# Optimization experiments

Measured on AMD Instinct MI355X. Metric: run time of the kernel, lower is better.

Reference implementation:

```python
import jax, jax.numpy as jnp
import numpy as np

SEQ, NV, NH, NR = 32768, 256, 512, 256


def _bern(key, p):
    # torch.bernoulli: sample is non-differentiable
    return (jax.random.uniform(key, p.shape, dtype=p.dtype) < p).astype(p.dtype)


def setup_inputs() -> dict:
    key = jax.random.key(0)
    ks = jax.random.split(key, 8)
    f32 = jnp.float32
    return {
        "v_seq": (jax.random.uniform(ks[0], (SEQ, NV), dtype=f32) < 0.1).astype(f32),
        "W1": jax.random.normal(ks[1], (NV, NH), dtype=f32) * 0.01,
        "bv": jnp.zeros((NV,), f32),
        "bh1": jnp.zeros((NH,), f32),
        "W2": jax.random.normal(ks[2], (NH, NH), dtype=f32) * 0.01,
        "bh2": jnp.zeros((NH,), f32),
        "Wyv": jax.random.normal(ks[3], (NV, NR), dtype=f32) * 1e-4,
        "Wyh1": jax.random.normal(ks[4], (NH, NR), dtype=f32) * 1e-4,
        "Wyh2": jax.random.normal(ks[5], (NH, NR), dtype=f32) * 1e-4,
        "Wvu": jax.random.normal(ks[6], (NV, NR), dtype=f32) * 0.01,
        "Wuu": jax.random.normal(ks[7], (NR, NR), dtype=f32) * 0.01,
        "bu": jnp.zeros((NR,), f32),
        "k": 5,
    }


def reference(v_seq, W1, bv, bh1, W2, bh2, Wyv, Wyh1, Wyh2, Wvu, Wuu, bu, k):
    dtype = v_seq.dtype
    nr = Wuu.shape[0]
    seq_len = v_seq.shape[0]

    # vanilla tanh RNN (abstract _run_rnn in base class)
    def rnn_step(u, v):
        u_new = jnp.tanh(v @ Wvu + u @ Wuu + bu)
        return u_new, u_new

    _, rnn_out = jax.lax.scan(rnn_step, jnp.zeros((nr,), dtype), v_seq)
    shifted = jnp.concatenate([jnp.zeros((1, nr), dtype), rnn_out[:-1]], axis=0)

    bv_t = bv + shifted @ Wyv.T    # [S, NV]
    bh1_t = bh1 + shifted @ Wyh1.T  # [S, NH]
    bh2_t = bh2 + shifted @ Wyh2.T  # [S, NH]

    key = jax.random.key(42)

    # CD-k Gibbs chain, RBM1 (visible <-> hidden1)
    v_sample = v_seq
    mean_v = None
    for _ in range(k):
        key, k1, k2 = jax.random.split(key, 3)
        h = _bern(k1, jax.nn.sigmoid(v_sample @ W1 + bh1_t))
        mean_v = jax.nn.sigmoid(h @ W1.T + bv_t)
        v_sample = _bern(k2, mean_v)

    def free_energy1(v):
        return -(v * bv_t).sum(-1) - jax.nn.softplus(v @ W1 + bh1_t).sum(-1)

    cost1 = (free_energy1(v_seq) - free_energy1(jax.lax.stop_gradient(v_sample))).mean()

    # CD-k Gibbs chain, RBM2 (hidden1 <-> hidden2)
    h1 = jax.nn.sigmoid(v_seq @ W1 + bh1_t)
    h1_sample = h1
    for _ in range(k):
        key, k1, k2 = jax.random.split(key, 3)
        h2 = _bern(k1, jax.nn.sigmoid(h1_sample @ W2 + bh2_t))
        h1_sample = _bern(k2, jax.nn.sigmoid(h2 @ W2.T + bh1_t))

    def free_energy2(h):
        return -(h * bh1_t).sum(-1) - jax.nn.softplus(h @ W2 + bh2_t).sum(-1)

    cost2 = (free_energy2(h1) - free_energy2(jax.lax.stop_gradient(h1_sample))).mean()

    eps = 1e-10
    monitor = (v_seq * jnp.log(mean_v + eps)
               + (1.0 - v_seq) * jnp.log(1.0 - mean_v + eps)).sum() / seq_len
    return (cost1 + cost2, monitor)
```

## Files before the change

kernel.cpp:

```cpp
#include <hip/hip_runtime.h>
#include <cstdint>

#define S_LEN 32768
#define NV 256
#define NH 512
#define NR 256

typedef short bf16x8 __attribute__((ext_vector_type(8)));
typedef float f32x4 __attribute__((ext_vector_type(4)));
typedef unsigned short ushort_t;

__device__ __forceinline__ float b2f(ushort_t u) {
  return __uint_as_float(((uint32_t)u) << 16);
}
__device__ __forceinline__ ushort_t f2b(float f) {
  uint32_t x = __float_as_uint(f);
  uint32_t r = (x + 0x7fffu + ((x >> 16) & 1u)) >> 16;
  return (ushort_t)r;
}

#define GLOAD_LDS16(gsrc, ldst)                                        \
  __builtin_amdgcn_global_load_lds(                                    \
      (const __attribute__((address_space(1))) void*)(gsrc),           \
      (__attribute__((address_space(3))) void*)(ldst), 16, 0, 0)

#define TFR(x0,x1,r) { x0 += x1; x1 = ((x1 << (r)) | (x1 >> (32 - (r)))); x1 ^= x0; }
__host__ __forceinline__ void tf2x32(uint32_t k0, uint32_t k1,
                                     uint32_t x0, uint32_t x1,
                                     uint32_t* o0, uint32_t* o1) {
  uint32_t k2 = k0 ^ k1 ^ 0x1BD11BDAu;
  x0 += k0; x1 += k1;
  TFR(x0,x1,13) TFR(x0,x1,15) TFR(x0,x1,26) TFR(x0,x1,6)
  x0 += k1; x1 += k2 + 1u;
  TFR(x0,x1,17) TFR(x0,x1,29) TFR(x0,x1,16) TFR(x0,x1,24)
  x0 += k2; x1 += k0 + 2u;
  TFR(x0,x1,13) TFR(x0,x1,15) TFR(x0,x1,26) TFR(x0,x1,6)
  x0 += k0; x1 += k1 + 3u;
  TFR(x0,x1,17) TFR(x0,x1,29) TFR(x0,x1,16) TFR(x0,x1,24)
  x0 += k1; x1 += k2 + 4u;
  TFR(x0,x1,13) TFR(x0,x1,15) TFR(x0,x1,26) TFR(x0,x1,6)
  x0 += k2; x1 += k0 + 5u;
  *o0 = x0; *o1 = x1;
}

__device__ __forceinline__ uint32_t fast_hash(uint32_t k0, uint32_t k1, uint32_t idx) {
  uint32_t h = idx ^ k0;
  h *= 0xCC9E2D51u; h = (h << 15) | (h >> 17); h *= 0x1B873593u;
  h ^= k1;
  h ^= h >> 16; h *= 0x85EBCA6Bu;
  h ^= h >> 13; h *= 0xC2B2AE35u;
  h ^= h >> 16;
  return h;
}

__device__ __forceinline__ float wave_reduce(float v) {
#pragma unroll
  for (int o = 32; o > 0; o >>= 1) v += __shfl_down(v, o, 64);
  return v;
}
__device__ __forceinline__ float softplusf(float z) {
  return fmaxf(z, 0.f) + log1pf(expf(-fabsf(z)));
}

#define F_SAMP  4
#define F_H1    8
#define F_FE    16
#define F_MON   32
#define F_DOTB  64
#define F_DOTS  128
#define F_DOTV  256

struct GemmArgs {
  const ushort_t* A;
  const ushort_t* BT;
  const ushort_t* Ax;
  const ushort_t* BXT;
  const float* bvec;
  ushort_t* C;
  ushort_t* C2;
  const float* vseqf;
  double* fe_acc;
  double* mon_acc;
  float sign;
  uint32_t rk0, rk1;
  int N, K, nbx;
};

__device__ __forceinline__ void xcd_swz(int* bx, int* by) {
  const int gx = (int)gridDim.x;
  const int lin = (int)blockIdx.y * gx + (int)blockIdx.x;
  const int cpx = (gx * (int)gridDim.y) >> 3;
  const int w = (lin & 7) * cpx + (lin >> 3);
  const int lg = 31 - __clz(gx);
  *by = w >> lg;
  *bx = w & (gx - 1);
}

template<int FLAGS>
__device__ __forceinline__ void run_gemm(const GemmArgs& g, int bx, int by,
                                         ushort_t* __restrict__ As0,
                                         ushort_t* __restrict__ As1,
                                         ushort_t* __restrict__ Bs0,
                                         ushort_t* __restrict__ Bs1) {
  constexpr bool HASB = (FLAGS & (F_DOTB | F_DOTS | F_DOTV)) != 0;
  const int tid = threadIdx.x;
  const int lane = tid & 63, wave = tid >> 6;
  const int wm = wave >> 1, wn = wave & 1;
  const int q = lane >> 4, l16 = lane & 15;
  const int m0 = by * 128, n0 = bx * 128;
  const int N = g.N, K = g.K;
  const int KT = K + 256;

  f32x4 acc[4][4];
  f32x4 accB[4][4];
#pragma unroll
  for (int mt = 0; mt < 4; mt++)
#pragma unroll
    for (int nt = 0; nt < 4; nt++) {
      acc[mt][nt] = (f32x4){0.f, 0.f, 0.f, 0.f};
      if constexpr (HASB) accB[mt][nt] = (f32x4){0.f, 0.f, 0.f, 0.f};
    }

  auto stage = [&](ushort_t* As, ushort_t* Bs, int kks) {
    const ushort_t* Ap; const ushort_t* Bp; size_t lda; int k0;
    if (kks < K) { Ap = g.A;  Bp = g.BT;  lda = (size_t)K; k0 = kks; }
    else         { Ap = g.Ax; Bp = g.BXT; lda = 256;       k0 = kks - K; }
#pragma unroll
    for (int j = 0; j < 4; j++) {
      int c = j * 256 + tid;
      int r = c >> 3, bl = c & 7, bg = bl ^ (r & 7);
      (void)bl;
      const int ldso = (j * 256 + wave * 64) * 8;
      GLOAD_LDS16(&Ap[(size_t)(m0 + r) * lda + k0 + bg * 8], &As[ldso]);
      GLOAD_LDS16(&Bp[(size_t)(n0 + r) * lda + k0 + bg * 8], &Bs[ldso]);
    }
  };
  auto compute_into = [&](f32x4 (&ac)[4][4], const ushort_t* As, const ushort_t* Bs) {
#pragma unroll
    for (int c = 0; c < 2; c++) {
      bf16x8 af[4], bf[4];
#pragma unroll
      for (int mt = 0; mt < 4; mt++) {
        int r = wm * 64 + mt * 16 + l16;
        af[mt] = *(const bf16x8*)&As[r * 64 + (((c * 4 + q) ^ (r & 7)) * 8)];
      }
#pragma unroll
      for (int nt = 0; nt < 4; nt++) {
        int r = wn * 64 + nt * 16 + l16;
        bf[nt] = *(const bf16x8*)&Bs[r * 64 + (((c * 4 + q) ^ (r & 7)) * 8)];
      }
#pragma unroll
      for (int mt = 0; mt < 4; mt++)
#pragma unroll
        for (int nt = 0; nt < 4; nt++)
          ac[mt][nt] = __builtin_amdgcn_mfma_f32_16x16x32_bf16(
              af[mt], bf[nt], ac[mt][nt], 0, 0, 0);
    }
  };

  stage(As0, Bs0, 0);
  __syncthreads();
  for (int kk = 0; kk < KT; kk += 128) {
    stage(As1, Bs1, kk + 64);
    if (HASB && kk >= K) compute_into(accB, As0, Bs0);
    else                 compute_into(acc,  As0, Bs0);
    __syncthreads();
    if (kk + 128 < KT) stage(As0, Bs0, kk + 128);
    if (HASB && (kk + 64) >= K) compute_into(accB, As1, Bs1);
    else                        compute_into(acc,  As1, Bs1);
    __syncthreads();
  }

  float fe_sum = 0.f, mon_sum = 0.f;
#pragma unroll
  for (int mt = 0; mt < 4; mt++) {
#pragma unroll
    for (int nt = 0; nt < 4; nt++) {
      const int gn = n0 + wn * 64 + nt * 16 + l16;
      const int gmb = m0 + wm * 64 + mt * 16 + q * 4;
      const float bvv = g.bvec[gn];
      uint32_t h0 = 0, h1 = 0;
      if constexpr (FLAGS & F_SAMP) {
        uint32_t pb = (uint32_t)((gmb >> 1) * N + gn);
        h0 = fast_hash(g.rk0, g.rk1, pb);
        h1 = fast_hash(g.rk0, g.rk1, pb + (uint32_t)N);
      }
#pragma unroll
      for (int rg = 0; rg < 4; rg++) {
        const int gm = gmb + rg;
        const size_t idx = (size_t)gm * N + gn;
        float z, be = 0.f;
        if constexpr (HASB) {
          be = accB[mt][nt][rg] + bvv;
          z = acc[mt][nt][rg] + be;
        } else {
          z = acc[mt][nt][rg] + bvv;
        }
        if constexpr (FLAGS & F_DOTV) fe_sum += be * g.vseqf[idx];
        if constexpr (FLAGS & (F_SAMP | F_H1 | F_MON)) {
          float e = __expf(-z);
          if constexpr (FLAGS & F_SAMP) {
            uint32_t hb = (rg & 2) ? h1 : h0;
            uint32_t ub = (rg & 1) ? (hb >> 16) : (hb & 0xffffu);
            float uu = (float)ub * (1.0f / 65536.0f);
            bool sbit = fmaf(uu, e, uu) < 1.f;
            g.C[idx] = sbit ? (ushort_t)0x3f80 : (ushort_t)0;
            if constexpr (FLAGS & F_DOTS) fe_sum += sbit ? be : 0.f;
          }
          if constexpr (FLAGS & (F_H1 | F_MON)) {
            float pp = __builtin_amdgcn_rcpf(1.f + e);
            if constexpr (FLAGS & F_H1) g.C2[idx] = f2b(pp);
            if constexpr (FLAGS & F_DOTB) fe_sum += pp * be;
            if constexpr (FLAGS & F_MON) {
              float v = g.vseqf[idx];
              mon_sum += (v != 0.f) ? logf(pp + 1e-10f) : logf(1.f - pp + 1e-10f);
            }
          }
        }
        if constexpr (FLAGS & F_FE) fe_sum += softplusf(z);
      }
    }
  }
  if constexpr (FLAGS & (F_FE | F_DOTB | F_DOTS | F_DOTV)) {
    float s = wave_reduce(fe_sum);
    if (lane == 0) atomicAdd(g.fe_acc, (double)(-g.sign * s));
  }
  if constexpr (FLAGS & F_MON) {
    float s = wave_reduce(mon_sum);
    if (lane == 0) atomicAdd(g.mon_acc, (double)s);
  }
}

template<int FLAGS>
__global__ __launch_bounds__(256)
void gemm_samp(GemmArgs g) {
  __shared__ ushort_t As0[128 * 64], As1[128 * 64];
  __shared__ ushort_t Bs0[128 * 64], Bs1[128 * 64];
  int bx, by;
  xcd_swz(&bx, &by);
  if (bx >= g.nbx) return;
  run_gemm<FLAGS>(g, bx, by, As0, As1, Bs0, Bs1);
}

template<int F0, int F1>
__global__ __launch_bounds__(256)
void gemm_pair(GemmArgs g0, GemmArgs g1) {
  __shared__ ushort_t As0[128 * 64], As1[128 * 64];
  __shared__ ushort_t Bs0[128 * 64], Bs1[128 * 64];
  int bx, by;
  xcd_swz(&bx, &by);
  if (blockIdx.z == 0) {
    if (bx >= g0.nbx) return;
    run_gemm<F0>(g0, bx, by, As0, As1, Bs0, Bs1);
  } else {
    if (bx >= g1.nbx) return;
    run_gemm<F1>(g1, bx, by, As0, As1, Bs0, Bs1);
  }
}

__global__ __launch_bounds__(256)
void gemm_bias(const ushort_t* __restrict__ A, const ushort_t* __restrict__ BT,
               const float* __restrict__ biasv, float* __restrict__ Cf,
               int M, int N, int K) {
  __shared__ ushort_t As0[128 * 64], As1[128 * 64];
  __shared__ ushort_t Bs0[128 * 64], Bs1[128 * 64];
  const int tid = threadIdx.x;
  const int lane = tid & 63, wave = tid >> 6;
  const int wm = wave >> 1, wn = wave & 1;
  const int q = lane >> 4, l16 = lane & 15;
  int bx, by;
  xcd_swz(&bx, &by);
  const int m0 = by * 128, n0 = bx * 128;
  (void)lane;

  f32x4 acc[4][4];
#pragma unroll
  for (int i = 0; i < 4; i++)
#pragma unroll
    for (int j = 0; j < 4; j++) acc[i][j] = (f32x4){0.f, 0.f, 0.f, 0.f};

  auto stage = [&](ushort_t* As, ushort_t* Bs, int kk) {
#pragma unroll
    for (int j = 0; j < 4; j++) {
      int c = j * 256 + tid;
      int r = c >> 3, bl = c & 7, bg = bl ^ (r & 7);
      (void)bl;
      const int ldso = (j * 256 + wave * 64) * 8;
      GLOAD_LDS16(&A[(size_t)(m0 + r) * K + kk + bg * 8], &As[ldso]);
      GLOAD_LDS16(&BT[(size_t)(n0 + r) * K + kk + bg * 8], &Bs[ldso]);
    }
  };
  auto compute = [&](const ushort_t* As, const ushort_t* Bs) {
#pragma unroll
    for (int c = 0; c < 2; c++) {
      bf16x8 af[4], bf[4];
#pragma unroll
      for (int mt = 0; mt < 4; mt++) {
        int r = wm * 64 + mt * 16 + l16;
        af[mt] = *(const bf16x8*)&As[r * 64 + (((c * 4 + q) ^ (r & 7)) * 8)];
      }
#pragma unroll
      for (int nt = 0; nt < 4; nt++) {
        int r = wn * 64 + nt * 16 + l16;
        bf[nt] = *(const bf16x8*)&Bs[r * 64 + (((c * 4 + q) ^ (r & 7)) * 8)];
      }
#pragma unroll
      for (int mt = 0; mt < 4; mt++)
#pragma unroll
        for (int nt = 0; nt < 4; nt++)
          acc[mt][nt] = __builtin_amdgcn_mfma_f32_16x16x32_bf16(
              af[mt], bf[nt], acc[mt][nt], 0, 0, 0);
    }
  };

  stage(As0, Bs0, 0);
  __syncthreads();
  for (int kk = 0; kk < K; kk += 128) {
    stage(As1, Bs1, kk + 64);
    compute(As0, Bs0);
    __syncthreads();
    if (kk + 128 < K) stage(As0, Bs0, kk + 128);
    compute(As1, Bs1);
    __syncthreads();
  }

#pragma unroll
  for (int mt = 0; mt < 4; mt++)
#pragma unroll
    for (int nt = 0; nt < 4; nt++) {
      const int gn = n0 + wn * 64 + nt * 16 + l16;
      const int gmb = m0 + wm * 64 + mt * 16 + q * 4;
      const float bvv = biasv[gn];
#pragma unroll
      for (int rg = 0; rg < 4; rg++)
        Cf[(size_t)(gmb + rg) * N + gn] = acc[mt][nt][rg] + bvv;
    }
}

__global__ __launch_bounds__(1024, 1)
void rnn_scan(const float* __restrict__ Apre, const float* __restrict__ Wuu,
              ushort_t* __restrict__ shifted) {
  const int tid = threadIdx.x;
  const int j = tid >> 2;
  const int s = tid & 3;
  const int t_begin = blockIdx.x * 128;
  const int t_end = t_begin + 128;
  const int t0 = (t_begin >= 16) ? (t_begin - 16) : 0;

  float w[64];
#pragma unroll
  for (int i = 0; i < 64; i++) w[i] = Wuu[(size_t)(s * 64 + i) * 256 + j];

  __shared__ float u[2][280];
  __shared__ float asg[32 * 256];
  if (tid < 256) u[0][(tid >> 6) * 68 + (tid & 63)] = 0.f;
  if (blockIdx.x == 0 && s == 0) shifted[j] = 0;
  __syncthreads();

  const int jp = (j >> 6) * 68 + (j & 63);
  int p = 0;
  for (int tb = t0; tb < t_end; tb += 32) {
    int srow = tb + (tid >> 5);
    if (srow >= S_LEN) srow = S_LEN - 1;
    int scol = (tid & 31) * 8;
    float4 a0 = *(const float4*)&Apre[(size_t)srow * 256 + scol];
    float4 a1 = *(const float4*)&Apre[(size_t)srow * 256 + scol + 4];
    *(float4*)&asg[(tid >> 5) * 256 + scol] = a0;
    *(float4*)&asg[(tid >> 5) * 256 + scol + 4] = a1;
    __syncthreads();
#pragma unroll 1
    for (int i = 0; i < 32; i++) {
      const int t = tb + i;
      if (t >= t_end) break;
      float p0 = 0.f, p1 = 0.f, p2 = 0.f, p3 = 0.f;
#pragma unroll
      for (int qq = 0; qq < 64; qq += 4) {
        float4 uv = *(const float4*)&u[p][s * 68 + qq];
        p0 = fmaf(uv.x, w[qq + 0], p0);
        p1 = fmaf(uv.y, w[qq + 1], p1);
        p2 = fmaf(uv.z, w[qq + 2], p2);
        p3 = fmaf(uv.w, w[qq + 3], p3);
      }
      float ps = (p0 + p1) + (p2 + p3);
      ps += __shfl_xor(ps, 1, 64);
      ps += __shfl_xor(ps, 2, 64);
      float z = asg[i * 256 + j] + ps;
      float e = __expf(2.f * z);
      float unew = 1.f - 2.f * __builtin_amdgcn_rcpf(e + 1.f);
      if (s == 0) {
        u[1 - p][jp] = unew;
        if (t >= t_begin && (t + 1) < S_LEN)
          shifted[(size_t)(t + 1) * 256 + j] = f2b(unew);
      }
      __syncthreads();
      p ^= 1;
    }
  }
}

__global__ __launch_bounds__(256)
void prep_all(const float* __restrict__ v_seq, ushort_t* __restrict__ vseq_bf,
              const float* __restrict__ Wyv, const float* __restrict__ Wyh1,
              const float* __restrict__ Wyh2, ushort_t* __restrict__ Wycat,
              const float* __restrict__ W1, ushort_t* __restrict__ BTw1t,
              ushort_t* __restrict__ BTw1,
              const float* __restrict__ W2, ushort_t* __restrict__ BTw2t,
              ushort_t* __restrict__ BTw2,
              const float* __restrict__ Wvu, ushort_t* __restrict__ BTwvu,
              const float* __restrict__ bv, const float* __restrict__ bh1,
              const float* __restrict__ bh2, float* __restrict__ bveccat) {
  int b = blockIdx.x;
  const int tid = threadIdx.x;
  if (b < 32768) { int i = b * 256 + tid; vseq_bf[i] = f2b(v_seq[i]); return; }
  b -= 32768;
  if (b < 256)  { int i = b * 256 + tid; Wycat[i] = f2b(Wyv[i]); return; }
  b -= 256;
  if (b < 512)  { int i = b * 256 + tid; Wycat[65536 + i] = f2b(Wyh1[i]); return; }
  b -= 512;
  if (b < 512)  { int i = b * 256 + tid; Wycat[196608 + i] = f2b(Wyh2[i]); return; }
  b -= 512;
  if (b < 512)  { int i = b * 256 + tid; BTw1t[i] = f2b(W1[i]); return; }
  b -= 512;
  if (b < 1024) { int i = b * 256 + tid; BTw2t[i] = f2b(W2[i]); return; }
  b -= 1024;
  if (b < 256)  { int i = b * 256 + tid; int r = i >> 8, c = i & 255;
                  BTwvu[c * 256 + r] = f2b(Wvu[i]); return; }
  b -= 256;
  if (b < 512)  { int i = b * 256 + tid; int r = i >> 9, c = i & 511;
                  BTw1[(size_t)c * 256 + r] = f2b(W1[i]); return; }
  b -= 512;
  if (b < 1024) { int i = b * 256 + tid; int r = i >> 9, c = i & 511;
                  BTw2[(size_t)c * 512 + r] = f2b(W2[i]); return; }
  b -= 1024;
  { int i = b * 256 + tid;
    if (i < 1280)
      bveccat[i] = (i < 256) ? bv[i] : (i < 768) ? bh1[i - 256] : bh2[i - 768]; }
}

__global__ void finalize_kernel(const double* __restrict__ acc, float* __restrict__ out) {
  out[0] = (float)(acc[0] / (double)S_LEN);
  out[1] = (float)(acc[1] / (double)S_LEN);
}

extern "C" void kernel_launch(void* const* d_in, const int* in_sizes, int n_in,
                              void* d_out, int out_size, void* d_ws, size_t ws_size,
                              hipStream_t stream) {
  (void)in_sizes; (void)n_in; (void)out_size; (void)ws_size;
  const float* v_seq = (const float*)d_in[0];
  const float* W1    = (const float*)d_in[1];
  const float* bv    = (const float*)d_in[2];
  const float* bh1   = (const float*)d_in[3];
  const float* W2    = (const float*)d_in[4];
  const float* bh2   = (const float*)d_in[5];
  const float* Wyv   = (const float*)d_in[6];
  const float* Wyh1  = (const float*)d_in[7];
  const float* Wyh2  = (const float*)d_in[8];
  const float* Wvu   = (const float*)d_in[9];
  const float* Wuu   = (const float*)d_in[10];
  const float* bu    = (const float*)d_in[11];
  float* out = (float*)d_out;

  const size_t SN = (size_t)S_LEN * NV;
  const size_t SH = (size_t)S_LEN * NH;
  char* base = (char*)d_ws;
  size_t cur = 0;
  auto take = [&](size_t bytes) { size_t o = cur; cur += (bytes + 255) & ~(size_t)255; return o; };
  double*   acc      = (double*)  (base + take(64));
  ushort_t* BTwvu    = (ushort_t*)(base + take(65536 * 2));
  ushort_t* Wycat    = (ushort_t*)(base + take((size_t)1280 * NR * 2));
  float*    bveccat  = (float*)   (base + take(1280 * 4));
  ushort_t* BTw1     = (ushort_t*)(base + take(131072 * 2));
  ushort_t* BTw1t    = (ushort_t*)(base + take(131072 * 2));
  ushort_t* BTw2     = (ushort_t*)(base + take(262144 * 2));
  ushort_t* BTw2t    = (ushort_t*)(base + take(262144 * 2));
  ushort_t* vseq_bf  = (ushort_t*)(base + take(SN * 2));
  ushort_t* shifted  = (ushort_t*)(base + take(SN * 2));
  float*    Arnn     = (float*)   (base + take(SN * 4));
  ushort_t* h1buf    = (ushort_t*)(base + take(SH * 2));
  ushort_t* sampA    = (ushort_t*)(base + take(SH * 2));
  ushort_t* sampB    = (ushort_t*)(base + take(SN * 2));
  ushort_t* sampC    = (ushort_t*)(base + take(SH * 2));
  ushort_t* sampD = h1buf;

  uint32_t ka[20], kb[20];
  uint32_t K0 = 0u, K1 = 42u;
  for (int it = 0; it < 10; it++) {
    uint32_t n0, n1, a0, a1, b0, b1;
    tf2x32(K0, K1, 0u, 0u, &n0, &n1);
    tf2x32(K0, K1, 0u, 1u, &a0, &a1);
    tf2x32(K0, K1, 0u, 2u, &b0, &b1);
    ka[2 * it] = a0; kb[2 * it] = a1;
    ka[2 * it + 1] = b0; kb[2 * it + 1] = b1;
    K0 = n0; K1 = n1;
  }

  hipMemsetAsync(acc, 0, 2 * sizeof(double), stream);

  dim3 blk(256);
  prep_all<<<dim3(37381), blk, 0, stream>>>(
      v_seq, vseq_bf, Wyv, Wyh1, Wyh2, Wycat, W1, BTw1t, BTw1,
      W2, BTw2t, BTw2, Wvu, BTwvu, bv, bh1, bh2, bveccat);

  const int M = S_LEN;
  gemm_bias<<<dim3(2, M / 128), blk, 0, stream>>>(
      vseq_bf, BTwvu, bu, Arnn, M, NV, NV);
  rnn_scan<<<dim3(S_LEN / 128), dim3(1024), 0, stream>>>(Arnn, Wuu, shifted);

  const int OFF_BV = 0, OFF_BH1 = NV, OFF_BH2 = NV + NH;
  auto mk = [&](const ushort_t* A, const ushort_t* BT, int boff, ushort_t* C,
                ushort_t* C2, const float* vs, float sign, int key, int N, int K) {
    GemmArgs g;
    g.A = A; g.BT = BT;
    g.Ax = shifted;
    g.BXT = Wycat + (size_t)boff * 256;
    g.bvec = bveccat + boff;
    g.C = C; g.C2 = C2; g.vseqf = vs;
    g.fe_acc = acc; g.mon_acc = acc + 1; g.sign = sign;
    g.rk0 = key >= 0 ? ka[key] : 0; g.rk1 = key >= 0 ? kb[key] : 0;
    g.N = N; g.K = K; g.nbx = N / 128;
    return g;
  };

  gemm_samp<F_SAMP | F_H1 | F_FE | F_DOTB>
      <<<dim3(4, M / 128), blk, 0, stream>>>(
      mk(vseq_bf, BTw1, OFF_BH1, sampA, h1buf, nullptr, 1.0f, 0, NH, NV));

  dim3 pg(4, M / 128, 2);
  GemmArgs V[5], Hh[4], A2g[5], B2g[5];
  for (int it = 0; it < 5; it++) {
    if (it > 0)
      Hh[it - 1] = mk(sampB, BTw1, OFF_BH1, sampA, nullptr, nullptr, 0.f,
                      2 * it, NH, NV);
    V[it] = mk(sampA, BTw1t, OFF_BV, sampB, nullptr,
               (it == 4 || it == 0) ? v_seq : nullptr,
               (it == 4) ? -1.0f : (it == 0) ? 1.0f : 0.f,
               2 * it + 1, NV, NH);
    A2g[it] = mk((it == 0) ? h1buf : sampD,
                 BTw2, OFF_BH2, sampC, nullptr, nullptr,
                 (it == 0) ? 1.0f : 0.f, 10 + 2 * it, NH, NH);
    B2g[it] = mk(sampC, BTw2t, OFF_BH1, sampD, nullptr, nullptr,
                 (it == 4) ? -1.0f : 0.f, 11 + 2 * it, NH, NH);
  }
  GemmArgs FE1 = mk(sampB, BTw1, OFF_BH1, nullptr, nullptr, nullptr, -1.0f,
                    -1, NH, NV);
  GemmArgs FE2 = mk(sampD, BTw2, OFF_BH2, nullptr, nullptr, nullptr, -1.0f,
                    -1, NH, NH);

  gemm_pair<F_SAMP | F_DOTV, F_SAMP | F_FE>
      <<<pg, blk, 0, stream>>>(V[0], A2g[0]);
  gemm_pair<F_SAMP, F_SAMP>
      <<<pg, blk, 0, stream>>>(Hh[0], B2g[0]);
  gemm_pair<F_SAMP, F_SAMP>
      <<<pg, blk, 0, stream>>>(V[1], A2g[1]);
  gemm_pair<F_SAMP, F_SAMP>
      <<<pg, blk, 0, stream>>>(Hh[1], B2g[1]);
  gemm_pair<F_SAMP, F_SAMP>
      <<<pg, blk, 0, stream>>>(V[2], A2g[2]);
  gemm_pair<F_SAMP, F_SAMP>
      <<<pg, blk, 0, stream>>>(Hh[2], B2g[2]);
  gemm_pair<F_SAMP, F_SAMP>
      <<<pg, blk, 0, stream>>>(V[3], A2g[3]);
  gemm_pair<F_SAMP, F_SAMP>
      <<<pg, blk, 0, stream>>>(Hh[3], B2g[3]);
  gemm_pair<F_SAMP | F_MON | F_DOTS, F_SAMP>
      <<<pg, blk, 0, stream>>>(V[4], A2g[4]);
  gemm_pair<F_FE, F_SAMP | F_DOTS>
      <<<pg, blk, 0, stream>>>(FE1, B2g[4]);

  gemm_samp<F_FE><<<dim3(4, M / 128), blk, 0, stream>>>(FE2);

  finalize_kernel<<<1, 1, 0, stream>>>(acc, out);
}
```

Before: 1.429 ms.

## Drop LDS double buffering and move bias-dot terms into separate dot_bias kernels

Replaces the double-buffered LDS pipeline in every GEMM with a single-buffer load-sync-compute loop. The free-energy dot terms against the time-varying biases no longer use a second accumulator inside the sampling GEMMs; two new dot_bias kernels compute them afterwards. Paired GEMMs now share one 2D grid instead of a z dimension, and sampD gets its own buffer. Halving LDS and dropping accB may raise occupancy, at the cost of losing load/compute overlap and recomputing the shifted@Wy products in extra launches.

```diff
diff --git a/kernel.cpp b/kernel.cpp
--- a/kernel.cpp
+++ b/kernel.cpp
@@ -66,9 +66,6 @@
 #define F_H1    8
 #define F_FE    16
 #define F_MON   32
-#define F_DOTB  64
-#define F_DOTS  128
-#define F_DOTV  256
 
 struct GemmArgs {
   const ushort_t* A;
@@ -89,20 +86,17 @@
 __device__ __forceinline__ void xcd_swz(int* bx, int* by) {
   const int gx = (int)gridDim.x;
   const int lin = (int)blockIdx.y * gx + (int)blockIdx.x;
-  const int cpx = (gx * (int)gridDim.y) >> 3;
+  const int cpx = (gx << 8) >> 3;
   const int w = (lin & 7) * cpx + (lin >> 3);
-  const int lg = 31 - __clz(gx);
-  *by = w >> lg;
-  *bx = w & (gx - 1);
+  const int byv = w / gx;
+  *by = __builtin_amdgcn_readfirstlane(byv);
+  *bx = __builtin_amdgcn_readfirstlane(w - byv * gx);
 }
 
 template<int FLAGS>
 __device__ __forceinline__ void run_gemm(const GemmArgs& g, int bx, int by,
-                                         ushort_t* __restrict__ As0,
-                                         ushort_t* __restrict__ As1,
-                                         ushort_t* __restrict__ Bs0,
-                                         ushort_t* __restrict__ Bs1) {
-  constexpr bool HASB = (FLAGS & (F_DOTB | F_DOTS | F_DOTV)) != 0;
+                                         ushort_t* __restrict__ As,
+                                         ushort_t* __restrict__ Bs) {
   const int tid = threadIdx.x;
   const int lane = tid & 63, wave = tid >> 6;
   const int wm = wave >> 1, wn = wave & 1;
@@ -112,30 +106,24 @@
   const int KT = K + 256;
 
   f32x4 acc[4][4];
-  f32x4 accB[4][4];
 #pragma unroll
   for (int mt = 0; mt < 4; mt++)
 #pragma unroll
-    for (int nt = 0; nt < 4; nt++) {
-      acc[mt][nt] = (f32x4){0.f, 0.f, 0.f, 0.f};
-      if constexpr (HASB) accB[mt][nt] = (f32x4){0.f, 0.f, 0.f, 0.f};
-    }
-
-  auto stage = [&](ushort_t* As, ushort_t* Bs, int kks) {
+    for (int nt = 0; nt < 4; nt++) acc[mt][nt] = (f32x4){0.f, 0.f, 0.f, 0.f};
+
+  for (int kk = 0; kk < KT; kk += 64) {
     const ushort_t* Ap; const ushort_t* Bp; size_t lda; int k0;
-    if (kks < K) { Ap = g.A;  Bp = g.BT;  lda = (size_t)K; k0 = kks; }
-    else         { Ap = g.Ax; Bp = g.BXT; lda = 256;       k0 = kks - K; }
+    if (kk < K) { Ap = g.A;  Bp = g.BT;  lda = (size_t)K; k0 = kk; }
+    else        { Ap = g.Ax; Bp = g.BXT; lda = 256;       k0 = kk - K; }
 #pragma unroll
     for (int j = 0; j < 4; j++) {
       int c = j * 256 + tid;
-      int r = c >> 3, bl = c & 7, bg = bl ^ (r & 7);
-      (void)bl;
+      int r = c >> 3, bg = (c & 7) ^ (r & 7);
       const int ldso = (j * 256 + wave * 64) * 8;
       GLOAD_LDS16(&Ap[(size_t)(m0 + r) * lda + k0 + bg * 8], &As[ldso]);
       GLOAD_LDS16(&Bp[(size_t)(n0 + r) * lda + k0 + bg * 8], &Bs[ldso]);
     }
-  };
-  auto compute_into = [&](f32x4 (&ac)[4][4], const ushort_t* As, const ushort_t* Bs) {
+    __syncthreads();
 #pragma unroll
     for (int c = 0; c < 2; c++) {
       bf16x8 af[4], bf[4];
@@ -153,21 +141,9 @@
       for (int mt = 0; mt < 4; mt++)
 #pragma unroll
         for (int nt = 0; nt < 4; nt++)
-          ac[mt][nt] = __builtin_amdgcn_mfma_f32_16x16x32_bf16(
-              af[mt], bf[nt], ac[mt][nt], 0, 0, 0);
-    }
-  };
-
-  stage(As0, Bs0, 0);
-  __syncthreads();
-  for (int kk = 0; kk < KT; kk += 128) {
-    stage(As1, Bs1, kk + 64);
-    if (HASB && kk >= K) compute_into(accB, As0, Bs0);
-    else                 compute_into(acc,  As0, Bs0);
-    __syncthreads();
-    if (kk + 128 < KT) stage(As0, Bs0, kk + 128);
-    if (HASB && (kk + 64) >= K) compute_into(accB, As1, Bs1);
-    else                        compute_into(acc,  As1, Bs1);
+          acc[mt][nt] = __builtin_amdgcn_mfma_f32_16x16x32_bf16(
+              af[mt], bf[nt], acc[mt][nt], 0, 0, 0);
+    }
     __syncthreads();
   }
 
@@ -189,14 +165,7 @@
       for (int rg = 0; rg < 4; rg++) {
         const int gm = gmb + rg;
         const size_t idx = (size_t)gm * N + gn;
-        float z, be = 0.f;
-        if constexpr (HASB) {
-          be = accB[mt][nt][rg] + bvv;
-          z = acc[mt][nt][rg] + be;
-        } else {
-          z = acc[mt][nt][rg] + bvv;
-        }
-        if constexpr (FLAGS & F_DOTV) fe_sum += be * g.vseqf[idx];
+        float z = acc[mt][nt][rg] + bvv;
         if constexpr (FLAGS & (F_SAMP | F_H1 | F_MON)) {
           float e = __expf(-z);
           if constexpr (FLAGS & F_SAMP) {
@@ -205,12 +174,10 @@
             float uu = (float)ub * (1.0f / 65536.0f);
             bool sbit = fmaf(uu, e, uu) < 1.f;
             g.C[idx] = sbit ? (ushort_t)0x3f80 : (ushort_t)0;
-            if constexpr (FLAGS & F_DOTS) fe_sum += sbit ? be : 0.f;
           }
           if constexpr (FLAGS & (F_H1 | F_MON)) {
             float pp = __builtin_amdgcn_rcpf(1.f + e);
             if constexpr (FLAGS & F_H1) g.C2[idx] = f2b(pp);
-            if constexpr (FLAGS & F_DOTB) fe_sum += pp * be;
             if constexpr (FLAGS & F_MON) {
               float v = g.vseqf[idx];
               mon_sum += (v != 0.f) ? logf(pp + 1e-10f) : logf(1.f - pp + 1e-10f);
@@ -221,7 +188,7 @@
       }
     }
   }
-  if constexpr (FLAGS & (F_FE | F_DOTB | F_DOTS | F_DOTV)) {
+  if constexpr (FLAGS & F_FE) {
     float s = wave_reduce(fe_sum);
     if (lane == 0) atomicAdd(g.fe_acc, (double)(-g.sign * s));
   }
@@ -234,36 +201,110 @@
 template<int FLAGS>
 __global__ __launch_bounds__(256)
 void gemm_samp(GemmArgs g) {
-  __shared__ ushort_t As0[128 * 64], As1[128 * 64];
-  __shared__ ushort_t Bs0[128 * 64], Bs1[128 * 64];
+  __shared__ ushort_t As[128 * 64];
+  __shared__ ushort_t Bs[128 * 64];
   int bx, by;
   xcd_swz(&bx, &by);
   if (bx >= g.nbx) return;
-  run_gemm<FLAGS>(g, bx, by, As0, As1, Bs0, Bs1);
+  run_gemm<FLAGS>(g, bx, by, As, Bs);
 }
 
 template<int F0, int F1>
 __global__ __launch_bounds__(256)
 void gemm_pair(GemmArgs g0, GemmArgs g1) {
-  __shared__ ushort_t As0[128 * 64], As1[128 * 64];
-  __shared__ ushort_t Bs0[128 * 64], Bs1[128 * 64];
+  __shared__ ushort_t As[128 * 64];
+  __shared__ ushort_t Bs[128 * 64];
   int bx, by;
   xcd_swz(&bx, &by);
-  if (blockIdx.z == 0) {
-    if (bx >= g0.nbx) return;
-    run_gemm<F0>(g0, bx, by, As0, As1, Bs0, Bs1);
+  if (bx < g0.nbx) {
+    run_gemm<F0>(g0, bx, by, As, Bs);
   } else {
-    if (bx >= g1.nbx) return;
-    run_gemm<F1>(g1, bx, by, As0, As1, Bs0, Bs1);
-  }
+    run_gemm<F1>(g1, bx - g0.nbx, by, As, Bs);
+  }
+}
+
+template<bool X2F32>
+__global__ __launch_bounds__(256)
+void dot_bias(const ushort_t* __restrict__ Ash, const ushort_t* __restrict__ BXT,
+              const float* __restrict__ bvec, const ushort_t* __restrict__ X1,
+              const void* __restrict__ X2, double* __restrict__ fe_acc, int N) {
+  __shared__ ushort_t As[128 * 64];
+  __shared__ ushort_t Bs[128 * 64];
+  const int tid = threadIdx.x;
+  const int lane = tid & 63, wave = tid >> 6;
+  const int wm = wave >> 1, wn = wave & 1;
+  const int q = lane >> 4, l16 = lane & 15;
+  int bx, by;
+  xcd_swz(&bx, &by);
+  const int m0 = by * 128, n0 = bx * 128;
+
+  f32x4 acc[4][4];
+#pragma unroll
+  for (int i = 0; i < 4; i++)
+#pragma unroll
+    for (int j = 0; j < 4; j++) acc[i][j] = (f32x4){0.f, 0.f, 0.f, 0.f};
+
+  for (int kk = 0; kk < 256; kk += 64) {
+#pragma unroll
+    for (int j = 0; j < 4; j++) {
+      int c = j * 256 + tid;
+      int r = c >> 3, bg = (c & 7) ^ (r & 7);
+      const int ldso = (j * 256 + wave * 64) * 8;
+      GLOAD_LDS16(&Ash[(size_t)(m0 + r) * 256 + kk + bg * 8], &As[ldso]);
+      GLOAD_LDS16(&BXT[(size_t)(n0 + r) * 256 + kk + bg * 8], &Bs[ldso]);
+    }
+    __syncthreads();
+#pragma unroll
+    for (int c = 0; c < 2; c++) {
+      bf16x8 af[4], bf[4];
+#pragma unroll
+      for (int mt = 0; mt < 4; mt++) {
+        int r = wm * 64 + mt * 16 + l16;
+        af[mt] = *(const bf16x8*)&As[r * 64 + (((c * 4 + q) ^ (r & 7)) * 8)];
+      }
+#pragma unroll
+      for (int nt = 0; nt < 4; nt++) {
+        int r = wn * 64 + nt * 16 + l16;
+        bf[nt] = *(const bf16x8*)&Bs[r * 64 + (((c * 4 + q) ^ (r & 7)) * 8)];
+      }
+#pragma unroll
+      for (int mt = 0; mt < 4; mt++)
+#pragma unroll
+        for (int nt = 0; nt < 4; nt++)
+          acc[mt][nt] = __builtin_amdgcn_mfma_f32_16x16x32_bf16(
+              af[mt], bf[nt], acc[mt][nt], 0, 0, 0);
+    }
+    __syncthreads();
+  }
+
+  float fe_sum = 0.f;
+#pragma unroll
+  for (int mt = 0; mt < 4; mt++)
+#pragma unroll
+    for (int nt = 0; nt < 4; nt++) {
+      const int gn = n0 + wn * 64 + nt * 16 + l16;
+      const int gmb = m0 + wm * 64 + mt * 16 + q * 4;
+      const float bvv = bvec[gn];
+#pragma unroll
+      for (int rg = 0; rg < 4; rg++) {
+        const size_t idx = (size_t)(gmb + rg) * N + gn;
+        float be = acc[mt][nt][rg] + bvv;
+        float x1 = b2f(X1[idx]);
+        float x2 = X2F32 ? ((const float*)X2)[idx]
+                         : b2f(((const ushort_t*)X2)[idx]);
+        fe_sum += be * (x1 - x2);
+      }
+    }
+  float s = wave_reduce(fe_sum);
+  if (lane == 0) atomicAdd(fe_acc, (double)s);
 }
 
 __global__ __launch_bounds__(256)
 void gemm_bias(const ushort_t* __restrict__ A, const ushort_t* __restrict__ BT,
                const float* __restrict__ biasv, float* __restrict__ Cf,
                int M, int N, int K) {
-  __shared__ ushort_t As0[128 * 64], As1[128 * 64];
-  __shared__ ushort_t Bs0[128 * 64], Bs1[128 * 64];
+  __shared__ ushort_t As[128 * 64];
+  __shared__ ushort_t Bs[128 * 64];
   const int tid = threadIdx.x;
   const int lane = tid & 63, wave = tid >> 6;
   const int wm = wave >> 1, wn = wave & 1;
@@ -279,18 +320,16 @@
 #pragma unroll
     for (int j = 0; j < 4; j++) acc[i][j] = (f32x4){0.f, 0.f, 0.f, 0.f};
 
-  auto stage = [&](ushort_t* As, ushort_t* Bs, int kk) {
+  for (int kk = 0; kk < K; kk += 64) {
 #pragma unroll
     for (int j = 0; j < 4; j++) {
       int c = j * 256 + tid;
-      int r = c >> 3, bl = c & 7, bg = bl ^ (r & 7);
-      (void)bl;
+      int r = c >> 3, bg = (c & 7) ^ (r & 7);
       const int ldso = (j * 256 + wave * 64) * 8;
       GLOAD_LDS16(&A[(size_t)(m0 + r) * K + kk + bg * 8], &As[ldso]);
       GLOAD_LDS16(&BT[(size_t)(n0 + r) * K + kk + bg * 8], &Bs[ldso]);
     }
-  };
-  auto compute = [&](const ushort_t* As, const ushort_t* Bs) {
+    __syncthreads();
 #pragma unroll
     for (int c = 0; c < 2; c++) {
       bf16x8 af[4], bf[4];
@@ -311,16 +350,6 @@
           acc[mt][nt] = __builtin_amdgcn_mfma_f32_16x16x32_bf16(
               af[mt], bf[nt], acc[mt][nt], 0, 0, 0);
     }
-  };
-
-  stage(As0, Bs0, 0);
-  __syncthreads();
-  for (int kk = 0; kk < K; kk += 128) {
-    stage(As1, Bs1, kk + 64);
-    compute(As0, Bs0);
-    __syncthreads();
-    if (kk + 128 < K) stage(As0, Bs0, kk + 128);
-    compute(As1, Bs1);
     __syncthreads();
   }
 
@@ -480,7 +509,7 @@
   ushort_t* sampA    = (ushort_t*)(base + take(SH * 2));
   ushort_t* sampB    = (ushort_t*)(base + take(SN * 2));
   ushort_t* sampC    = (ushort_t*)(base + take(SH * 2));
-  ushort_t* sampD = h1buf;
+  ushort_t* sampD    = (ushort_t*)(base + take(SH * 2));
 
   uint32_t ka[20], kb[20];
   uint32_t K0 = 0u, K1 = 42u;
@@ -521,53 +550,61 @@
     return g;
   };
 
-  gemm_samp<F_SAMP | F_H1 | F_FE | F_DOTB>
+  gemm_samp<F_SAMP | F_H1 | F_FE>
       <<<dim3(4, M / 128), blk, 0, stream>>>(
       mk(vseq_bf, BTw1, OFF_BH1, sampA, h1buf, nullptr, 1.0f, 0, NH, NV));
 
-  dim3 pg(4, M / 128, 2);
   GemmArgs V[5], Hh[4], A2g[5], B2g[5];
   for (int it = 0; it < 5; it++) {
     if (it > 0)
       Hh[it - 1] = mk(sampB, BTw1, OFF_BH1, sampA, nullptr, nullptr, 0.f,
                       2 * it, NH, NV);
     V[it] = mk(sampA, BTw1t, OFF_BV, sampB, nullptr,
-               (it == 4 || it == 0) ? v_seq : nullptr,
-               (it == 4) ? -1.0f : (it == 0) ? 1.0f : 0.f,
-               2 * it + 1, NV, NH);
+               (it == 4) ? v_seq : nullptr, 0.f, 2 * it + 1, NV, NH);
     A2g[it] = mk((it == 0) ? h1buf : sampD,
                  BTw2, OFF_BH2, sampC, nullptr, nullptr,
                  (it == 0) ? 1.0f : 0.f, 10 + 2 * it, NH, NH);
-    B2g[it] = mk(sampC, BTw2t, OFF_BH1, sampD, nullptr, nullptr,
-                 (it == 4) ? -1.0f : 0.f, 11 + 2 * it, NH, NH);
+    B2g[it] = mk(sampC, BTw2t, OFF_BH1, sampD, nullptr, nullptr, 0.f,
+                 11 + 2 * it, NH, NH);
   }
   GemmArgs FE1 = mk(sampB, BTw1, OFF_BH1, nullptr, nullptr, nullptr, -1.0f,
                     -1, NH, NV);
   GemmArgs FE2 = mk(sampD, BTw2, OFF_BH2, nullptr, nullptr, nullptr, -1.0f,
                     -1, NH, NH);
 
-  gemm_pair<F_SAMP | F_DOTV, F_SAMP | F_FE>
-      <<<pg, blk, 0, stream>>>(V[0], A2g[0]);
+  auto pgrid = [&](const GemmArgs& a, const GemmArgs& b) {
+    return dim3(a.nbx + b.nbx, M / 128);
+  };
+
+  gemm_pair<F_SAMP, F_SAMP | F_FE>
+      <<<pgrid(V[0], A2g[0]), blk, 0, stream>>>(V[0], A2g[0]);
   gemm_pair<F_SAMP, F_SAMP>
-      <<<pg, blk, 0, stream>>>(Hh[0], B2g[0]);
+      <<<pgrid(Hh[0], B2g[0]), blk, 0, stream>>>(Hh[0], B2g[0]);
   gemm_pair<F_SAMP, F_SAMP>
-      <<<pg, blk, 0, stream>>>(V[1], A2g[1]);
+      <<<pgrid(V[1], A2g[1]), blk, 0, stream>>>(V[1], A2g[1]);
   gemm_pair<F_SAMP, F_SAMP>
-      <<<pg, blk, 0, stream>>>(Hh[1], B2g[1]);
+      <<<pgrid(Hh[1], B2g[1]), blk, 0, stream>>>(Hh[1], B2g[1]);
   gemm_pair<F_SAMP, F_SAMP>
-      <<<pg, blk, 0, stream>>>(V[2], A2g[2]);
+      <<<pgrid(V[2], A2g[2]), blk, 0, stream>>>(V[2], A2g[2]);
   gemm_pair<F_SAMP, F_SAMP>
-      <<<pg, blk, 0, stream>>>(Hh[2], B2g[2]);
+      <<<pgrid(Hh[2], B2g[2]), blk, 0, stream>>>(Hh[2], B2g[2]);
   gemm_pair<F_SAMP, F_SAMP>
-      <<<pg, blk, 0, stream>>>(V[3], A2g[3]);
+      <<<pgrid(V[3], A2g[3]), blk, 0, stream>>>(V[3], A2g[3]);
   gemm_pair<F_SAMP, F_SAMP>
-      <<<pg, blk, 0, stream>>>(Hh[3], B2g[3]);
-  gemm_pair<F_SAMP | F_MON | F_DOTS, F_SAMP>
-      <<<pg, blk, 0, stream>>>(V[4], A2g[4]);
-  gemm_pair<F_FE, F_SAMP | F_DOTS>
-      <<<pg, blk, 0, stream>>>(FE1, B2g[4]);
+      <<<pgrid(Hh[3], B2g[3]), blk, 0, stream>>>(Hh[3], B2g[3]);
+  gemm_pair<F_SAMP | F_MON, F_SAMP>
+      <<<pgrid(V[4], A2g[4]), blk, 0, stream>>>(V[4], A2g[4]);
+  gemm_pair<F_FE, F_SAMP>
+      <<<pgrid(FE1, B2g[4]), blk, 0, stream>>>(FE1, B2g[4]);
 
   gemm_samp<F_FE><<<dim3(4, M / 128), blk, 0, stream>>>(FE2);
 
+  dot_bias<true><<<dim3(2, M / 128), blk, 0, stream>>>(
+      shifted, Wycat + (size_t)OFF_BV * 256, bveccat + OFF_BV,
+      sampB, v_seq, acc, NV);
+  dot_bias<false><<<dim3(4, M / 128), blk, 0, stream>>>(
+      shifted, Wycat + (size_t)OFF_BH1 * 256, bveccat + OFF_BH1,
+      sampD, h1buf, acc, NH);
+
   finalize_kernel<<<1, 1, 0, stream>>>(acc, out);
 }
```

Result: faster. 1.185 ms (median of 2 runs) (-17.1%).
